# Kernel optimization log

Measured on AMD Instinct MI355X. Metric: run time of the kernel, lower is better.

Reference implementation:

```python
import jax, jax.numpy as jnp
import numpy as np

B, S, D, H = 4, 2048, 1024, 16
Dh = D // H


def _layernorm(x, a, b):
    # torch.var default is unbiased (ddof=1)
    mu = jnp.mean(x, axis=-1, keepdims=True)
    sg = jnp.var(x, axis=-1, keepdims=True, ddof=1)
    return (x - mu) / jnp.sqrt(sg + 1e-08) * a + b


def setup_inputs() -> dict:
    key = jax.random.key(0)
    ks = jax.random.split(key, 16)
    s = 1.0 / np.sqrt(D)
    inp = {
        'q': jax.random.normal(ks[0], (B, S, D), jnp.float32),
        'k': jax.random.normal(ks[1], (B, S, D), jnp.float32),
        'v': jax.random.normal(ks[2], (B, S, D), jnp.float32),
        'g': jax.random.normal(ks[3], (B, S, D), jnp.float32),
        # causal mask: True = masked
        'm': jnp.triu(jnp.ones((S, S), jnp.bool_), k=1)[None, None],
        'Wq': jax.random.uniform(ks[4], (D, D), jnp.float32, -s, s),
        'bq': jnp.zeros((D,), jnp.float32),
        'Wk': jax.random.uniform(ks[5], (D, D), jnp.float32, -s, s),
        'bk': jnp.zeros((D,), jnp.float32),
        'Wv': jax.random.uniform(ks[6], (D, D), jnp.float32, -s, s),
        'bv': jnp.zeros((D,), jnp.float32),
        'Wg': jax.random.uniform(ks[7], (D, D), jnp.float32, -s, s),
        'bg': jnp.zeros((D,), jnp.float32),
        'ln_a': jnp.ones((D,), jnp.float32),
        'ln_b': jnp.zeros((D,), jnp.float32),
        'Wo': jax.random.uniform(ks[8], (D, D), jnp.float32, -s, s),
        'bo': jnp.zeros((D,), jnp.float32),
    }
    return inp


def reference(q, k, v, g, m, Wq, bq, Wk, bk, Wv, bv, Wg, bg, ln_a, ln_b, Wo, bo):
    qp = q @ Wq.T + bq
    kp = k @ Wk.T + bk
    vp = v @ Wv.T + bv
    gp = g @ Wg.T + bg
    # gating path: exact GELU (torch default), then custom LayerNorm (unbiased var)
    vp = jax.nn.gelu(vp, approximate=False)
    gp = jax.nn.gelu(gp, approximate=False)
    vp = _layernorm(vp, ln_a, ln_b)
    # [B,S,D] -> [B,H,S,Dh]
    qh = qp.reshape(B, S, H, Dh).transpose(0, 2, 1, 3)
    kh = kp.reshape(B, S, H, Dh).transpose(0, 2, 1, 3)
    vh = vp.reshape(B, S, H, Dh).transpose(0, 2, 1, 3)
    gh = gp.reshape(B, S, H, Dh).transpose(0, 2, 1, 3)
    a = jnp.einsum('bhqd,bhkd->bhqk', qh, kh) / jnp.sqrt(jnp.float32(Dh))
    a = jnp.where(m, -jnp.inf, a)
    a = jax.nn.softmax(a, axis=-1)
    # dropout = 0.0 (inference): no-op
    o = jnp.einsum('bhqk,bhkd->bhqd', a, vh)
    o = o * gh
    o = o.transpose(0, 2, 1, 3).reshape(B, S, D)
    o = o @ Wo.T + bo
    return (o, a)
```

## Files before the change

kernel.cpp:

```cpp
#include <hip/hip_runtime.h>
#include <hip/hip_bf16.h>
#include <cstdint>
#include <cstddef>

#define DEVINL static __device__ __forceinline__

typedef short bf16x8 __attribute__((ext_vector_type(8)));
typedef short s16x4  __attribute__((ext_vector_type(4)));
typedef float f32x4  __attribute__((ext_vector_type(4)));
typedef unsigned short u16;

static constexpr int Bb = 4, Ss = 2048, Dd = 1024, Hh = 16;
static constexpr int Mrows = Bb * Ss;
static constexpr int BHc = Bb * Hh;

DEVINL u16 f2bf(float f) {
    union { float f; uint32_t u; } v; v.f = f;
    uint32_t r = v.u + 0x7fffu + ((v.u >> 16) & 1u);
    return (u16)(r >> 16);
}
DEVINL float bf2f(u16 h) {
    union { uint32_t u; float f; } v; v.u = ((uint32_t)h) << 16;
    return v.f;
}
DEVINL uint32_t cvt_pk_bf16(float lo, float hi) {
    uint32_t r;
    asm("v_cvt_pk_bf16_f32 %0, %1, %2" : "=v"(r) : "v"(lo), "v"(hi));
    return r;
}
DEVINL float gelu_exact(float x) {
    return 0.5f * x * (1.0f + erff(x * 0.70710678118654752f));
}
DEVINL void gload16(const u16* gsrc, u16* ldsdst) {
    auto* g = reinterpret_cast<const __attribute__((address_space(1))) uint32_t*>(
        reinterpret_cast<uintptr_t>(gsrc));
    auto* l = reinterpret_cast<__attribute__((address_space(3))) uint32_t*>(
        reinterpret_cast<uintptr_t>(ldsdst));
    __builtin_amdgcn_global_load_lds(g, l, 16, 0, 0);
}

__global__ __launch_bounds__(256) void k_cvt_in(
    const float* __restrict__ s0, const float* __restrict__ s1,
    const float* __restrict__ s2, const float* __restrict__ s3,
    u16* __restrict__ d0, u16* __restrict__ d1,
    u16* __restrict__ d2, u16* __restrict__ d3, int n4) {
    int t = blockIdx.x * 256 + threadIdx.x;
    if (t >= n4) return;
    const float* s; u16* d;
    switch (blockIdx.y) {
        case 0: s = s0; d = d0; break;
        case 1: s = s1; d = d1; break;
        case 2: s = s2; d = d2; break;
        default: s = s3; d = d3; break;
    }
    float4 v = ((const float4*)s)[t];
    ushort4 o;
    o.x = f2bf(v.x); o.y = f2bf(v.y); o.z = f2bf(v.z); o.w = f2bf(v.w);
    ((ushort4*)d)[t] = o;
}

__global__ __launch_bounds__(256) void k_cvt_w(
    const float* __restrict__ s0, const float* __restrict__ s1,
    const float* __restrict__ s2, const float* __restrict__ s3,
    const float* __restrict__ s4,
    u16* __restrict__ d0, u16* __restrict__ d1, u16* __restrict__ d2,
    u16* __restrict__ d3, u16* __restrict__ d4, int n4) {
    int t = blockIdx.x * 256 + threadIdx.x;
    if (t >= n4) return;
    const float* s; u16* d;
    switch (blockIdx.y) {
        case 0: s = s0; d = d0; break;
        case 1: s = s1; d = d1; break;
        case 2: s = s2; d = d2; break;
        case 3: s = s3; d = d3; break;
        default: s = s4; d = d4; break;
    }
    float4 v = ((const float4*)s)[t];
    ushort4 o;
    o.x = f2bf(v.x); o.y = f2bf(v.y); o.z = f2bf(v.z); o.w = f2bf(v.w);
    ((ushort4*)d)[t] = o;
}

__global__ __launch_bounds__(512) void k_proj(
    const u16* __restrict__ qb, const u16* __restrict__ kb,
    const u16* __restrict__ vb, const u16* __restrict__ gb,
    const u16* __restrict__ Wqb, const u16* __restrict__ Wkb,
    const u16* __restrict__ Wvb, const u16* __restrict__ Wgb,
    const float* __restrict__ bqp, const float* __restrict__ bkp,
    const float* __restrict__ bvp, const float* __restrict__ bgp,
    u16* __restrict__ qp, u16* __restrict__ kpo,
    float* __restrict__ vp, u16* __restrict__ ghb)
{
    __shared__ u16 As[256 * 64];
    __shared__ u16 Bs[256 * 64];
    const int tid = threadIdx.x, lane = tid & 63, w = tid >> 6;
    const int wm = w >> 2, wn = w & 3;
    const int g = lane >> 4, li = lane & 15;
    const int orig = blockIdx.x;
    const int lid = (orig & 7) * 64 + (orig >> 3);
    const int z = lid >> 7, rem = lid & 127;
    const int m0 = (rem >> 2) * 256, n0 = (rem & 3) * 256;

    const u16 *Ap, *Wp; const float* bias;
    switch (z) {
        case 0: Ap = qb; Wp = Wqb; bias = bqp; break;
        case 1: Ap = kb; Wp = Wkb; bias = bkp; break;
        case 2: Ap = vb; Wp = Wvb; bias = bvp; break;
        default: Ap = gb; Wp = Wgb; bias = bgp; break;
    }

    const f32x4 zero4 = {0.f, 0.f, 0.f, 0.f};
    f32x4 acc[8][4];
#pragma unroll
    for (int mi = 0; mi < 8; mi++)
#pragma unroll
        for (int ni = 0; ni < 4; ni++) acc[mi][ni] = zero4;

    for (int k0 = 0; k0 < 1024; k0 += 64) {
        __syncthreads();
#pragma unroll
        for (int i = 0; i < 4; i++) {
            int u = i * 512 + w * 64 + lane;
            int row = u >> 3, cp = u & 7;
            gload16(Ap + (size_t)(m0 + row) * 1024 + k0 + ((cp ^ (row & 7)) << 3),
                    &As[(i * 512 + w * 64) * 8]);
        }
#pragma unroll
        for (int i = 0; i < 4; i++) {
            int u = i * 512 + w * 64 + lane;
            int row = u >> 3, cp = u & 7;
            gload16(Wp + (size_t)(n0 + row) * 1024 + k0 + ((cp ^ (row & 7)) << 3),
                    &Bs[(i * 512 + w * 64) * 8]);
        }
        __syncthreads();

#pragma unroll
        for (int kk2 = 0; kk2 < 2; kk2++) {
            bf16x8 af[8], bfr[4];
#pragma unroll
            for (int mi = 0; mi < 8; mi++) {
                int row = wm * 128 + mi * 16 + li;
                int lc = kk2 * 4 + g;
                af[mi] = *(const bf16x8*)&As[row * 64 + ((lc ^ (row & 7)) << 3)];
            }
#pragma unroll
            for (int ni = 0; ni < 4; ni++) {
                int row = wn * 64 + ni * 16 + li;
                int lc = kk2 * 4 + g;
                bfr[ni] = *(const bf16x8*)&Bs[row * 64 + ((lc ^ (row & 7)) << 3)];
            }
#pragma unroll
            for (int mi = 0; mi < 8; mi++)
#pragma unroll
                for (int ni = 0; ni < 4; ni++)
                    acc[mi][ni] = __builtin_amdgcn_mfma_f32_16x16x32_bf16(af[mi], bfr[ni], acc[mi][ni], 0, 0, 0);
        }
    }

#pragma unroll
    for (int mi = 0; mi < 8; mi++) {
#pragma unroll
        for (int ni = 0; ni < 4; ni++) {
            int col = n0 + wn * 64 + ni * 16 + li;
            float bv = bias[col];
#pragma unroll
            for (int r = 0; r < 4; r++) {
                int row = m0 + wm * 128 + mi * 16 + g * 4 + r;
                float v = acc[mi][ni][r] + bv;
                size_t idx = (size_t)row * 1024 + col;
                if (z == 0)      qp[idx]  = f2bf(v * 0.125f);
                else if (z == 1) kpo[idx] = f2bf(v);
                else if (z == 2) vp[idx]  = gelu_exact(v);
                else             ghb[idx] = f2bf(gelu_exact(v));
            }
        }
    }
}

__global__ __launch_bounds__(512) void k_gemm_f(
    const u16* __restrict__ Ap, const u16* __restrict__ Wp,
    const float* __restrict__ bias, float* __restrict__ Cp)
{
    __shared__ u16 As[256 * 64];
    __shared__ u16 Bs[256 * 64];
    const int tid = threadIdx.x, lane = tid & 63, w = tid >> 6;
    const int wm = w >> 2, wn = w & 3;
    const int g = lane >> 4, li = lane & 15;
    const int orig = blockIdx.x;
    const int lid = (orig & 7) * 16 + (orig >> 3);
    const int m0 = (lid >> 2) * 256, n0 = (lid & 3) * 256;

    const f32x4 zero4 = {0.f, 0.f, 0.f, 0.f};
    f32x4 acc[8][4];
#pragma unroll
    for (int mi = 0; mi < 8; mi++)
#pragma unroll
        for (int ni = 0; ni < 4; ni++) acc[mi][ni] = zero4;

    for (int k0 = 0; k0 < 1024; k0 += 64) {
        __syncthreads();
#pragma unroll
        for (int i = 0; i < 4; i++) {
            int u = i * 512 + w * 64 + lane;
            int row = u >> 3, cp = u & 7;
            gload16(Ap + (size_t)(m0 + row) * 1024 + k0 + ((cp ^ (row & 7)) << 3),
                    &As[(i * 512 + w * 64) * 8]);
        }
#pragma unroll
        for (int i = 0; i < 4; i++) {
            int u = i * 512 + w * 64 + lane;
            int row = u >> 3, cp = u & 7;
            gload16(Wp + (size_t)(n0 + row) * 1024 + k0 + ((cp ^ (row & 7)) << 3),
                    &Bs[(i * 512 + w * 64) * 8]);
        }
        __syncthreads();

#pragma unroll
        for (int kk2 = 0; kk2 < 2; kk2++) {
            bf16x8 af[8], bfr[4];
#pragma unroll
            for (int mi = 0; mi < 8; mi++) {
                int row = wm * 128 + mi * 16 + li;
                int lc = kk2 * 4 + g;
                af[mi] = *(const bf16x8*)&As[row * 64 + ((lc ^ (row & 7)) << 3)];
            }
#pragma unroll
            for (int ni = 0; ni < 4; ni++) {
                int row = wn * 64 + ni * 16 + li;
                int lc = kk2 * 4 + g;
                bfr[ni] = *(const bf16x8*)&Bs[row * 64 + ((lc ^ (row & 7)) << 3)];
            }
#pragma unroll
            for (int mi = 0; mi < 8; mi++)
#pragma unroll
                for (int ni = 0; ni < 4; ni++)
                    acc[mi][ni] = __builtin_amdgcn_mfma_f32_16x16x32_bf16(af[mi], bfr[ni], acc[mi][ni], 0, 0, 0);
        }
    }

#pragma unroll
    for (int mi = 0; mi < 8; mi++) {
#pragma unroll
        for (int ni = 0; ni < 4; ni++) {
            int col = n0 + wn * 64 + ni * 16 + li;
            float bv = bias[col];
#pragma unroll
            for (int r = 0; r < 4; r++) {
                int row = m0 + wm * 128 + mi * 16 + g * 4 + r;
                Cp[(size_t)row * 1024 + col] = acc[mi][ni][r] + bv;
            }
        }
    }
}

__global__ __launch_bounds__(256) void k_ln(const float* __restrict__ vp,
                                            const float* __restrict__ la,
                                            const float* __restrict__ lb,
                                            u16* __restrict__ vh) {
    int row = blockIdx.x;
    const float* x = vp + (size_t)row * 1024;
    int tid = threadIdx.x;
    float4 v = ((const float4*)x)[tid];
    float s = v.x + v.y + v.z + v.w;
    float s2 = v.x * v.x + v.y * v.y + v.z * v.z + v.w * v.w;
#pragma unroll
    for (int off = 1; off < 64; off <<= 1) {
        s  += __shfl_xor(s, off, 64);
        s2 += __shfl_xor(s2, off, 64);
    }
    __shared__ float red[8];
    int w = tid >> 6, lane = tid & 63;
    if (lane == 0) { red[w] = s; red[4 + w] = s2; }
    __syncthreads();
    s  = red[0] + red[1] + red[2] + red[3];
    s2 = red[4] + red[5] + red[6] + red[7];
    float mu = s * (1.0f / 1024.0f);
    float var = (s2 - 1024.0f * mu * mu) * (1.0f / 1023.0f);
    float rs = rsqrtf(var + 1e-8f);
    float4 a4 = ((const float4*)la)[tid];
    float4 b4 = ((const float4*)lb)[tid];
    ushort4 o;
    o.x = f2bf((v.x - mu) * rs * a4.x + b4.x);
    o.y = f2bf((v.y - mu) * rs * a4.y + b4.y);
    o.z = f2bf((v.z - mu) * rs * a4.z + b4.z);
    o.w = f2bf((v.w - mu) * rs * a4.w + b4.w);
    ((ushort4*)(vh + (size_t)row * 1024))[tid] = o;
}

__global__ __launch_bounds__(256) void k_transpose(const u16* __restrict__ vh,
                                                   u16* __restrict__ vhT) {
    int bh = blockIdx.y, b = bh >> 4, h = bh & 15, s0 = blockIdx.x * 64;
    __shared__ u16 t[64 * 96];
    int tid = threadIdx.x;
#pragma unroll
    for (int j = 0; j < 2; j++) {
        int u = j * 256 + tid;
        int r = u >> 3, c8 = u & 7;
        bf16x8 v = *(const bf16x8*)(vh + ((size_t)(b * 2048 + s0 + r) * 1024 + h * 64 + c8 * 8));
        *(bf16x8*)&t[r * 96 + c8 * 8] = v;
    }
    __syncthreads();
#pragma unroll
    for (int j = 0; j < 2; j++) {
        int u = j * 256 + tid;
        int d = u >> 3, s8 = u & 7;
        bf16x8 vv;
#pragma unroll
        for (int jj = 0; jj < 8; jj++) vv[jj] = (short)t[(s8 * 8 + jj) * 96 + d];
        *(bf16x8*)(vhT + ((size_t)(bh * 64 + d) * 2048 + s0 + s8 * 8)) = vv;
    }
}

__global__ __launch_bounds__(512) void k_attn(const u16* __restrict__ qp,
                                              const u16* __restrict__ kp,
                                              const u16* __restrict__ vhT,
                                              const u16* __restrict__ gh,
                                              float* __restrict__ aout,
                                              u16* __restrict__ gated) {
    __shared__ short Ps[8 * 16 * 128];
    const int tid = threadIdx.x, lane = tid & 63, w = tid >> 6;
    const int g = lane >> 4, li = lane & 15;
    const int orig = blockIdx.x;
    const int lid = (orig & 7) * 64 + (orig >> 3);
    const int bh = lid >> 3, i0 = lid & 7;
    const int b = bh >> 4, h = bh & 15;
    const u16* kbh = kp + ((size_t)(b * 2048) * 1024 + h * 64);
    const u16* vbh = vhT + (size_t)bh * 64 * 2048;
    const u16* ghb_base = gh + (size_t)(b * 2048) * 1024 + h * 64;
    float* arow = aout + (size_t)bh * 2048 * 2048;
    short* Pw = &Ps[w * 2048];
    const f32x4 zero4 = {0.f, 0.f, 0.f, 0.f};

    for (int half = 0; half < 2; ++half) {
        const int bx = half ? (15 - i0) : i0;
        const int q0 = bx * 128;
        const int qrow0 = q0 + w * 16;
        const int qrow = qrow0 + li;
        const u16* qbase = qp + ((size_t)(b * 2048 + qrow) * 1024 + h * 64 + g * 8);
        bf16x8 qa0 = *(const bf16x8*)qbase;
        bf16x8 qa1 = *(const bf16x8*)(qbase + 32);

        for (int kt = bx + 1; kt < 16; ++kt) {
            float* tbase = arow + (size_t)q0 * 2048 + kt * 128;
#pragma unroll
            for (int i = 0; i < 8; i++) {
                int u = i * 512 + tid;
                int row = u >> 5, cu = u & 31;
                __builtin_nontemporal_store(zero4, (f32x4*)(tbase + (size_t)row * 2048 + cu * 4));
            }
        }

        float l_run = 0.f;
        for (int kt = 0; kt <= bx; ++kt) {
            const int k0 = kt * 128;
            const bool full = (kt < bx);
#pragma unroll
            for (int n = 0; n < 8; n++) {
                int rb = k0 + n * 16 + li;
                const u16* krow = kbh + (size_t)rb * 1024 + g * 8;
                bf16x8 kb0 = *(const bf16x8*)krow;
                bf16x8 kb1 = *(const bf16x8*)(krow + 32);
                f32x4 c = zero4;
                c = __builtin_amdgcn_mfma_f32_16x16x32_bf16(kb0, qa0, c, 0, 0, 0);
                c = __builtin_amdgcn_mfma_f32_16x16x32_bf16(kb1, qa1, c, 0, 0, 0);
                if (full) {
#pragma unroll
                    for (int r = 0; r < 4; r++) l_run += __expf(c[r]);
                } else {
#pragma unroll
                    for (int r = 0; r < 4; r++) {
                        int col = k0 + n * 16 + g * 4 + r;
                        l_run += (col <= qrow) ? __expf(c[r]) : 0.0f;
                    }
                }
            }
        }
        l_run += __shfl_xor(l_run, 16, 64);
        l_run += __shfl_xor(l_run, 32, 64);
        const float linv = 1.0f / l_run;

        f32x4 oacc[4];
#pragma unroll
        for (int n = 0; n < 4; n++) oacc[n] = zero4;
        for (int kt = 0; kt <= bx; ++kt) {
            const int k0 = kt * 128;
            const bool full = (kt < bx);
#pragma unroll
            for (int n = 0; n < 8; n++) {
                int rb = k0 + n * 16 + li;
                const u16* krow = kbh + (size_t)rb * 1024 + g * 8;
                bf16x8 kb0 = *(const bf16x8*)krow;
                bf16x8 kb1 = *(const bf16x8*)(krow + 32);
                f32x4 c = zero4;
                c = __builtin_amdgcn_mfma_f32_16x16x32_bf16(kb0, qa0, c, 0, 0, 0);
                c = __builtin_amdgcn_mfma_f32_16x16x32_bf16(kb1, qa1, c, 0, 0, 0);
                if (full) {
#pragma unroll
                    for (int r = 0; r < 4; r++) c[r] = __expf(c[r]) * linv;
                } else {
#pragma unroll
                    for (int r = 0; r < 4; r++) {
                        int col = k0 + n * 16 + g * 4 + r;
                        c[r] = (col <= qrow) ? __expf(c[r]) * linv : 0.0f;
                    }
                }
                __builtin_nontemporal_store(c,
                    (f32x4*)(arow + (size_t)qrow * 2048 + k0 + n * 16 + g * 4));
                uint2 pk;
                pk.x = cvt_pk_bf16(c[0], c[1]);
                pk.y = cvt_pk_bf16(c[2], c[3]);
                int chunk = n * 2 + (g >> 1);
                *(uint2*)&Pw[li * 128 + ((chunk ^ (li & 7)) << 3) + (g & 1) * 4] = pk;
            }
#pragma unroll
            for (int ks = 0; ks < 4; ++ks) {
                int cl = ks * 4 + g;
                bf16x8 pa = *(const bf16x8*)&Pw[li * 128 + ((cl ^ (li & 7)) << 3)];
#pragma unroll
                for (int n = 0; n < 4; n++) {
                    int vr = n * 16 + li;
                    bf16x8 vb = *(const bf16x8*)(vbh + (size_t)vr * 2048 + k0 + cl * 8);
                    oacc[n] = __builtin_amdgcn_mfma_f32_16x16x32_bf16(pa, vb, oacc[n], 0, 0, 0);
                }
            }
        }

#pragma unroll
        for (int n = 0; n < 4; n++) {
            int d8 = n * 2 + (li >> 3), wi = li & 7;
#pragma unroll
            for (int r = 0; r < 4; r++) {
                int lr = g * 4 + r;
                Pw[lr * 64 + ((d8 ^ (lr & 7)) << 3) + wi] = (short)f2bf(oacc[n][r]);
            }
        }
#pragma unroll
        for (int it = 0; it < 2; ++it) {
            int lr = it * 8 + (lane >> 3);
            int c8 = lane & 7;
            int rowq = qrow0 + lr;
            bf16x8 ov = *(const bf16x8*)&Pw[lr * 64 + ((c8 ^ (lr & 7)) << 3)];
            bf16x8 gv = *(const bf16x8*)(ghb_base + (size_t)rowq * 1024 + c8 * 8);
            float p0 = bf2f((u16)ov[0]) * bf2f((u16)gv[0]);
            float p1 = bf2f((u16)ov[1]) * bf2f((u16)gv[1]);
            float p2 = bf2f((u16)ov[2]) * bf2f((u16)gv[2]);
            float p3 = bf2f((u16)ov[3]) * bf2f((u16)gv[3]);
            float p4 = bf2f((u16)ov[4]) * bf2f((u16)gv[4]);
            float p5 = bf2f((u16)ov[5]) * bf2f((u16)gv[5]);
            float p6 = bf2f((u16)ov[6]) * bf2f((u16)gv[6]);
            float p7 = bf2f((u16)ov[7]) * bf2f((u16)gv[7]);
            uint4 outv;
            outv.x = cvt_pk_bf16(p0, p1);
            outv.y = cvt_pk_bf16(p2, p3);
            outv.z = cvt_pk_bf16(p4, p5);
            outv.w = cvt_pk_bf16(p6, p7);
            *(uint4*)(gated + ((size_t)(b * 2048 + rowq)) * 1024 + h * 64 + c8 * 8) = outv;
        }
    }
}

extern "C" void kernel_launch(void* const* d_in, const int* in_sizes, int n_in,
                              void* d_out, int out_size, void* d_ws, size_t ws_size,
                              hipStream_t stream) {
    const float* q  = (const float*)d_in[0];
    const float* k  = (const float*)d_in[1];
    const float* v  = (const float*)d_in[2];
    const float* g  = (const float*)d_in[3];
    const float* Wq = (const float*)d_in[5];
    const float* bq = (const float*)d_in[6];
    const float* Wk = (const float*)d_in[7];
    const float* bk = (const float*)d_in[8];
    const float* Wv = (const float*)d_in[9];
    const float* bv = (const float*)d_in[10];
    const float* Wg = (const float*)d_in[11];
    const float* bg = (const float*)d_in[12];
    const float* ln_a = (const float*)d_in[13];
    const float* ln_b = (const float*)d_in[14];
    const float* Wo = (const float*)d_in[15];
    const float* bo = (const float*)d_in[16];

    float* o_out = (float*)d_out;
    float* a_out = o_out + (size_t)Mrows * Dd;

    u16* qp    = (u16*)d_ws;
    u16* kpb   = qp    + (size_t)Mrows * Dd;
    u16* vhT   = kpb   + (size_t)Mrows * Dd;
    u16* ghb   = vhT   + (size_t)Mrows * Dd;
    u16* gated = ghb   + (size_t)Mrows * Dd;
    u16* Wo_bf = gated + (size_t)Mrows * Dd;

    u16* Wq_bf = (u16*)a_out;
    u16* Wk_bf = Wq_bf + (size_t)Dd * Dd;
    u16* Wv_bf = Wk_bf + (size_t)Dd * Dd;
    u16* Wg_bf = Wv_bf + (size_t)Dd * Dd;
    u16* qb    = Wg_bf + (size_t)Dd * Dd;
    u16* kb2   = qb    + (size_t)Mrows * Dd;
    u16* vb    = kb2   + (size_t)Mrows * Dd;
    u16* gb    = vb    + (size_t)Mrows * Dd;
    float* vp  = (float*)(gb + (size_t)Mrows * Dd);
    u16* vh    = (u16*)(vp + (size_t)Mrows * Dd);

    {
        int n4w = Dd * Dd / 4;
        dim3 gw((n4w + 255) / 256, 5);
        k_cvt_w<<<gw, 256, 0, stream>>>(Wq, Wk, Wv, Wg, Wo,
                                        Wq_bf, Wk_bf, Wv_bf, Wg_bf, Wo_bf, n4w);
        int n4i = Mrows * Dd / 4;
        dim3 gi((n4i + 255) / 256, 4);
        k_cvt_in<<<gi, 256, 0, stream>>>(q, k, v, g, qb, kb2, vb, gb, n4i);
    }

    k_proj<<<512, 512, 0, stream>>>(qb, kb2, vb, gb,
                                    Wq_bf, Wk_bf, Wv_bf, Wg_bf,
                                    bq, bk, bv, bg,
                                    qp, kpb, vp, ghb);

    k_ln<<<Mrows, 256, 0, stream>>>(vp, ln_a, ln_b, vh);

    dim3 gt(Ss / 64, BHc);
    k_transpose<<<gt, 256, 0, stream>>>(vh, vhT);

    k_attn<<<512, 512, 0, stream>>>(qp, kpb, vhT, ghb, a_out, gated);

    k_gemm_f<<<128, 512, 0, stream>>>(gated, Wo_bf, bo, o_out);
}
```

Before: 721.3 us.

## Double-buffer LDS tiles in projection and output GEMMs to overlap loads

```diff
diff --git a/kernel.cpp b/kernel.cpp
--- a/kernel.cpp
+++ b/kernel.cpp
@@ -91,8 +91,8 @@
     u16* __restrict__ qp, u16* __restrict__ kpo,
     float* __restrict__ vp, u16* __restrict__ ghb)
 {
-    __shared__ u16 As[256 * 64];
-    __shared__ u16 Bs[256 * 64];
+    __shared__ u16 As[2][256 * 64];
+    __shared__ u16 Bs[2][256 * 64];
     const int tid = threadIdx.x, lane = tid & 63, w = tid >> 6;
     const int wm = w >> 2, wn = w & 3;
     const int g = lane >> 4, li = lane & 15;
@@ -109,6 +109,17 @@
         default: Ap = gb; Wp = Wgb; bias = bgp; break;
     }
 
+    size_t aoff[4], boff[4];
+    int ldst[4];
+#pragma unroll
+    for (int i = 0; i < 4; i++) {
+        int u = i * 512 + tid;
+        int row = u >> 3, cp = u & 7;
+        aoff[i] = (size_t)(m0 + row) * 1024 + ((cp ^ (row & 7)) << 3);
+        boff[i] = (size_t)(n0 + row) * 1024 + ((cp ^ (row & 7)) << 3);
+        ldst[i] = (i * 512 + w * 64) * 8;
+    }
+
     const f32x4 zero4 = {0.f, 0.f, 0.f, 0.f};
     f32x4 acc[8][4];
 #pragma unroll
@@ -116,24 +127,21 @@
 #pragma unroll
         for (int ni = 0; ni < 4; ni++) acc[mi][ni] = zero4;
 
-    for (int k0 = 0; k0 < 1024; k0 += 64) {
-        __syncthreads();
-#pragma unroll
-        for (int i = 0; i < 4; i++) {
-            int u = i * 512 + w * 64 + lane;
-            int row = u >> 3, cp = u & 7;
-            gload16(Ap + (size_t)(m0 + row) * 1024 + k0 + ((cp ^ (row & 7)) << 3),
-                    &As[(i * 512 + w * 64) * 8]);
-        }
-#pragma unroll
-        for (int i = 0; i < 4; i++) {
-            int u = i * 512 + w * 64 + lane;
-            int row = u >> 3, cp = u & 7;
-            gload16(Wp + (size_t)(n0 + row) * 1024 + k0 + ((cp ^ (row & 7)) << 3),
-                    &Bs[(i * 512 + w * 64) * 8]);
-        }
-        __syncthreads();
-
+#pragma unroll
+    for (int i = 0; i < 4; i++) gload16(Ap + aoff[i], &As[0][ldst[i]]);
+#pragma unroll
+    for (int i = 0; i < 4; i++) gload16(Wp + boff[i], &Bs[0][ldst[i]]);
+    __syncthreads();
+
+    for (int kt = 0; kt < 16; ++kt) {
+        const int cur = kt & 1;
+        if (kt < 15) {
+            const int k0n = (kt + 1) * 64;
+#pragma unroll
+            for (int i = 0; i < 4; i++) gload16(Ap + aoff[i] + k0n, &As[cur ^ 1][ldst[i]]);
+#pragma unroll
+            for (int i = 0; i < 4; i++) gload16(Wp + boff[i] + k0n, &Bs[cur ^ 1][ldst[i]]);
+        }
 #pragma unroll
         for (int kk2 = 0; kk2 < 2; kk2++) {
             bf16x8 af[8], bfr[4];
@@ -141,13 +149,13 @@
             for (int mi = 0; mi < 8; mi++) {
                 int row = wm * 128 + mi * 16 + li;
                 int lc = kk2 * 4 + g;
-                af[mi] = *(const bf16x8*)&As[row * 64 + ((lc ^ (row & 7)) << 3)];
+                af[mi] = *(const bf16x8*)&As[cur][row * 64 + ((lc ^ (row & 7)) << 3)];
             }
 #pragma unroll
             for (int ni = 0; ni < 4; ni++) {
                 int row = wn * 64 + ni * 16 + li;
                 int lc = kk2 * 4 + g;
-                bfr[ni] = *(const bf16x8*)&Bs[row * 64 + ((lc ^ (row & 7)) << 3)];
+                bfr[ni] = *(const bf16x8*)&Bs[cur][row * 64 + ((lc ^ (row & 7)) << 3)];
             }
 #pragma unroll
             for (int mi = 0; mi < 8; mi++)
@@ -155,6 +163,7 @@
                 for (int ni = 0; ni < 4; ni++)
                     acc[mi][ni] = __builtin_amdgcn_mfma_f32_16x16x32_bf16(af[mi], bfr[ni], acc[mi][ni], 0, 0, 0);
         }
+        __syncthreads();
     }
 
 #pragma unroll
@@ -181,8 +190,8 @@
     const u16* __restrict__ Ap, const u16* __restrict__ Wp,
     const float* __restrict__ bias, float* __restrict__ Cp)
 {
-    __shared__ u16 As[256 * 64];
-    __shared__ u16 Bs[256 * 64];
+    __shared__ u16 As[2][256 * 64];
+    __shared__ u16 Bs[2][256 * 64];
     const int tid = threadIdx.x, lane = tid & 63, w = tid >> 6;
     const int wm = w >> 2, wn = w & 3;
     const int g = lane >> 4, li = lane & 15;
@@ -190,6 +199,17 @@
     const int lid = (orig & 7) * 16 + (orig >> 3);
     const int m0 = (lid >> 2) * 256, n0 = (lid & 3) * 256;
 
+    size_t aoff[4], boff[4];
+    int ldst[4];
+#pragma unroll
+    for (int i = 0; i < 4; i++) {
+        int u = i * 512 + tid;
+        int row = u >> 3, cp = u & 7;
+        aoff[i] = (size_t)(m0 + row) * 1024 + ((cp ^ (row & 7)) << 3);
+        boff[i] = (size_t)(n0 + row) * 1024 + ((cp ^ (row & 7)) << 3);
+        ldst[i] = (i * 512 + w * 64) * 8;
+    }
+
     const f32x4 zero4 = {0.f, 0.f, 0.f, 0.f};
     f32x4 acc[8][4];
 #pragma unroll
@@ -197,24 +217,21 @@
 #pragma unroll
         for (int ni = 0; ni < 4; ni++) acc[mi][ni] = zero4;
 
-    for (int k0 = 0; k0 < 1024; k0 += 64) {
-        __syncthreads();
-#pragma unroll
-        for (int i = 0; i < 4; i++) {
-            int u = i * 512 + w * 64 + lane;
-            int row = u >> 3, cp = u & 7;
-            gload16(Ap + (size_t)(m0 + row) * 1024 + k0 + ((cp ^ (row & 7)) << 3),
-                    &As[(i * 512 + w * 64) * 8]);
-        }
-#pragma unroll
-        for (int i = 0; i < 4; i++) {
-            int u = i * 512 + w * 64 + lane;
-            int row = u >> 3, cp = u & 7;
-            gload16(Wp + (size_t)(n0 + row) * 1024 + k0 + ((cp ^ (row & 7)) << 3),
-                    &Bs[(i * 512 + w * 64) * 8]);
-        }
-        __syncthreads();
-
+#pragma unroll
+    for (int i = 0; i < 4; i++) gload16(Ap + aoff[i], &As[0][ldst[i]]);
+#pragma unroll
+    for (int i = 0; i < 4; i++) gload16(Wp + boff[i], &Bs[0][ldst[i]]);
+    __syncthreads();
+
+    for (int kt = 0; kt < 16; ++kt) {
+        const int cur = kt & 1;
+        if (kt < 15) {
+            const int k0n = (kt + 1) * 64;
+#pragma unroll
+            for (int i = 0; i < 4; i++) gload16(Ap + aoff[i] + k0n, &As[cur ^ 1][ldst[i]]);
+#pragma unroll
+            for (int i = 0; i < 4; i++) gload16(Wp + boff[i] + k0n, &Bs[cur ^ 1][ldst[i]]);
+        }
 #pragma unroll
         for (int kk2 = 0; kk2 < 2; kk2++) {
             bf16x8 af[8], bfr[4];
@@ -222,13 +239,13 @@
             for (int mi = 0; mi < 8; mi++) {
                 int row = wm * 128 + mi * 16 + li;
                 int lc = kk2 * 4 + g;
-                af[mi] = *(const bf16x8*)&As[row * 64 + ((lc ^ (row & 7)) << 3)];
+                af[mi] = *(const bf16x8*)&As[cur][row * 64 + ((lc ^ (row & 7)) << 3)];
             }
 #pragma unroll
             for (int ni = 0; ni < 4; ni++) {
                 int row = wn * 64 + ni * 16 + li;
                 int lc = kk2 * 4 + g;
-                bfr[ni] = *(const bf16x8*)&Bs[row * 64 + ((lc ^ (row & 7)) << 3)];
+                bfr[ni] = *(const bf16x8*)&Bs[cur][row * 64 + ((lc ^ (row & 7)) << 3)];
             }
 #pragma unroll
             for (int mi = 0; mi < 8; mi++)
@@ -236,6 +253,7 @@
                 for (int ni = 0; ni < 4; ni++)
                     acc[mi][ni] = __builtin_amdgcn_mfma_f32_16x16x32_bf16(af[mi], bfr[ni], acc[mi][ni], 0, 0, 0);
         }
+        __syncthreads();
     }
 
 #pragma unroll
```

Measured after the change: 682.2 us. 1.06x faster.
